# Kernel optimization log

Measured on AMD Instinct MI355X. Metric: run time of the kernel, lower is better.

## Reference

```python
import jax, jax.numpy as jnp
import numpy as np

N_TOKEN = 392
POS_WEIGHT = 1.0
LOSS_WEIGHT = 1.0


def _cam_map(logits, w_proj, xf, shape):
    # logits: (B, K_cls); w_proj: (K_cls, C); xf: (B, C, N)
    B, T, H, W = shape
    top_cls = jnp.argmax(logits, axis=1)                 # sort desc -> [0] == argmax
    w_top = w_proj[top_cls]                              # (B, C) gather top-class weight row
    row = jnp.einsum('bc,bcn->bn', w_top, xf)            # (B, N) per-sample CAM scores
    mn = row.min(axis=1, keepdims=True)
    mx = row.max(axis=1, keepdims=True)
    rown = (row - mn) / (mx - mn)                        # min-max normalize
    vals, idxs = jax.lax.top_k(rown, N_TOKEN)            # (B, 392)
    hw = H * W
    ti = idxs // hw
    hi = (idxs % hw) // W
    wi = idxs % W
    bi = jnp.broadcast_to(jnp.arange(B)[:, None], idxs.shape)
    cam = jnp.zeros((B, T, H, W), rown.dtype).at[bi, ti, hi, wi].set(vals)
    return cam


def _forward(x, pred_v_logits, pred_n_logits, w_proj_v, w_proj_n,
             conv_w, conv_b, score_w, score_b):
    B, C, T, H, W = x.shape
    xf = x.reshape(B, C, T * H * W)
    cam_v = _cam_map(pred_v_logits, w_proj_v, xf, (B, T, H, W))
    cam_n = _cam_map(pred_n_logits, w_proj_n, xf, (B, T, H, W))
    cam_gt = jnp.maximum(cam_v, cam_n)                   # torch.where(v > n, v, n)
    cam_gt = jax.lax.stop_gradient(cam_gt)               # original builds it from numpy + .detach()

    dn = ('NCDHW', 'OIDHW', 'NCDHW')
    h1 = jax.nn.relu(
        jax.lax.conv_general_dilated(x, conv_w, (1, 1, 1),
                                     [(0, 0), (1, 1), (1, 1)],
                                     dimension_numbers=dn)
        + conv_b[None, :, None, None, None])
    logits = (jax.lax.conv_general_dilated(h1, score_w, (1, 1, 1),
                                           [(0, 0), (0, 0), (0, 0)],
                                           dimension_numbers=dn)
              + score_b[None, :, None, None, None])      # (B,1,T,H,W)

    xcam = logits[:, 0].reshape(B * T, H * W)
    y = cam_gt.reshape(B * T, H * W)
    # BCEWithLogitsLoss(pos_weight) mean
    bce = -(POS_WEIGHT * y * jax.nn.log_sigmoid(xcam)
            + (1.0 - y) * jax.nn.log_sigmoid(-xcam))
    return LOSS_WEIGHT * bce.mean()


def setup_inputs() -> dict:
    key = jax.random.key(0)
    ks = jax.random.split(key, 8)
    B, C, T, H, W = 64, 256, 32, 7, 7
    Kv, Kn, D = 97, 300, 512
    x = jax.random.normal(ks[0], (B, C, T, H, W), jnp.float32)
    pred_v_logits = jax.random.normal(ks[1], (B, Kv), jnp.float32)
    pred_n_logits = jax.random.normal(ks[2], (B, Kn), jnp.float32)
    w_proj_v = jax.random.normal(ks[3], (Kv, C), jnp.float32) / np.sqrt(C)
    w_proj_n = jax.random.normal(ks[4], (Kn, C), jnp.float32) / np.sqrt(C)
    conv_w = jax.random.normal(ks[5], (D, C, 1, 3, 3), jnp.float32) / np.sqrt(C * 9)
    conv_b = jnp.zeros((D,), jnp.float32)
    score_w = jax.random.normal(ks[6], (1, D, 1, 1, 1), jnp.float32) / np.sqrt(D)
    score_b = jnp.zeros((1,), jnp.float32)
    return {"x": x, "pred_v_logits": pred_v_logits, "pred_n_logits": pred_n_logits,
            "w_proj_v": w_proj_v, "w_proj_n": w_proj_n,
            "conv_w": conv_w, "conv_b": conv_b,
            "score_w": score_w, "score_b": score_b}


def reference(x, pred_v_logits, pred_n_logits, w_proj_v, w_proj_n,
              conv_w, conv_b, score_w, score_b):
    return _forward(x, pred_v_logits, pred_n_logits, w_proj_v, w_proj_n,
                    conv_w, conv_b, score_w, score_b)
```

## Files before the change

kernel.cpp:

```cpp
#include <hip/hip_runtime.h>
#include <hip/hip_bf16.h>
#include <math.h>

#define BB 64
#define CC 256
#define TT 32
#define HH 7
#define WW 7
#define HW 49
#define NN 1568
#define KV 97
#define KN 300
#define DD 512
#define NTOK 392
#define TOTAL (BB*TT*HW)
#define BCAP 256

typedef float f32x4 __attribute__((ext_vector_type(4)));
typedef short bf16x8 __attribute__((ext_vector_type(8)));

#define GLDS(g, l) __builtin_amdgcn_global_load_lds(                          \
    (const __attribute__((address_space(1))) void*)(g),                       \
    (__attribute__((address_space(3))) void*)(l), 16, 0, 0)

__global__ void k_argmax(const float* __restrict__ pv, const float* __restrict__ pn,
                         int* __restrict__ clsv, int* __restrict__ clsn) {
    int b = threadIdx.x;
    if (b >= BB) return;
    {
        const float* r = pv + b * KV;
        float best = r[0]; int bi = 0;
        for (int k = 1; k < KV; ++k) { float v = r[k]; if (v > best) { best = v; bi = k; } }
        clsv[b] = bi;
    }
    {
        const float* r = pn + b * KN;
        float best = r[0]; int bi = 0;
        for (int k = 1; k < KN; ++k) { float v = r[k]; if (v > best) { best = v; bi = k; } }
        clsn[b] = bi;
    }
}

__global__ __launch_bounds__(256) void k_xp(
        const float* __restrict__ x, __hip_bfloat16* __restrict__ xp,
        const float* __restrict__ wpv, const float* __restrict__ wpn,
        const int* __restrict__ clsv, const int* __restrict__ clsn,
        float* __restrict__ rowv, float* __restrict__ rown_) {
    __shared__ float xs[CC * HW];
    __shared__ float wvs[CC], wns[CC];
    int bt = blockIdx.x;
    int b = bt >> 5, t = bt & 31;
    int tid = threadIdx.x;
    wvs[tid] = wpv[clsv[b] * CC + tid];
    wns[tid] = wpn[clsn[b] * CC + tid];
    const float* xb = x + ((size_t)b * CC * TT + t) * HW;
    for (int i = tid; i < CC * HW; i += 256) {
        int c = i / HW, q = i % HW;
        xs[i] = xb[(size_t)c * (TT * HW) + q];
    }
    __syncthreads();
    __hip_bfloat16* xpb = xp + (size_t)bt * 81 * CC;
    for (int o = tid; o < 81 * CC; o += 256) {
        int p = o >> 8, c = o & 255;
        int hh = p / 9, ww = p % 9;
        float v = 0.f;
        if (hh >= 1 && hh <= 7 && ww >= 1 && ww <= 7)
            v = xs[c * HW + (hh - 1) * WW + (ww - 1)];
        xpb[o] = __float2bfloat16(v);
    }
    if (tid < 2 * HW) {
        int head = tid >= HW;
        int q = head ? tid - HW : tid;
        const float* w = head ? wns : wvs;
        float s = 0.f;
        #pragma unroll 4
        for (int c = 0; c < CC; ++c) s = fmaf(w[c], xs[c * HW + q], s);
        (head ? rown_ : rowv)[bt * HW + q] = s;
    }
}

__global__ void k_wb(const float* __restrict__ w, __hip_bfloat16* __restrict__ wb) {
    int o = blockIdx.x * 256 + threadIdx.x;
    if (o >= 9 * DD * CC) return;
    int kk = o / (DD * CC);
    int rem = o - kk * (DD * CC);
    int d = rem >> 8, c = rem & 255;
    wb[o] = __float2bfloat16(w[(d * CC + c) * 9 + kk]);
}

__device__ __forceinline__ int binof(float v) {
    int i = (int)(v * 1024.f);
    return i < 0 ? 0 : (i > 1023 ? 1023 : i);
}

__device__ float block_red(float v, float* sbuf, int tid, bool ismax) {
    sbuf[tid] = v; __syncthreads();
    for (int s = 128; s > 0; s >>= 1) {
        if (tid < s) sbuf[tid] = ismax ? fmaxf(sbuf[tid], sbuf[tid + s])
                                       : fminf(sbuf[tid], sbuf[tid + s]);
        __syncthreads();
    }
    float r = sbuf[0]; __syncthreads();
    return r;
}

__global__ __launch_bounds__(256) void k_cam(
        const float* __restrict__ rowv, const float* __restrict__ rown_,
        float* __restrict__ cam) {
    __shared__ float rv[NN], rn[NN];
    __shared__ float sbuf[256];
    __shared__ int h[1024];
    __shared__ int tsum[256];
    __shared__ float lval_v[BCAP], lval_n[BCAP];
    __shared__ int lidx_v[BCAP], lidx_n[BCAP];
    __shared__ int cntv, cntn, bstar_v, above_v, bstar_n, above_n;
    int b = blockIdx.x, tid = threadIdx.x;

    for (int n = tid; n < NN; n += 256) { rv[n] = rowv[b * NN + n]; rn[n] = rown_[b * NN + n]; }
    __syncthreads();
    float mnv = 1e30f, mxv = -1e30f, mnn = 1e30f, mxn = -1e30f;
    for (int n = tid; n < NN; n += 256) {
        float v = rv[n]; mnv = fminf(mnv, v); mxv = fmaxf(mxv, v);
        float u = rn[n]; mnn = fminf(mnn, u); mxn = fmaxf(mxn, u);
    }
    mnv = block_red(mnv, sbuf, tid, false);
    mxv = block_red(mxv, sbuf, tid, true);
    mnn = block_red(mnn, sbuf, tid, false);
    mxn = block_red(mxn, sbuf, tid, true);
    float iv = 1.f / (mxv - mnv), inn = 1.f / (mxn - mnn);

    for (int n = tid; n < NN; n += 256) {
        rv[n] = (rv[n] - mnv) * iv;
        rn[n] = (rn[n] - mnn) * inn;
    }
    for (int i = tid; i < 1024; i += 256) h[i] = 0;
    if (tid == 0) { cntv = 0; cntn = 0; }
    __syncthreads();
    for (int n = tid; n < NN; n += 256) {
        atomicAdd(&h[binof(rv[n])], 1);
        atomicAdd(&h[binof(rn[n])], 1 << 16);
    }
    __syncthreads();

    int h0 = h[4 * tid], h1 = h[4 * tid + 1], h2 = h[4 * tid + 2], h3 = h[4 * tid + 3];
    tsum[tid] = h0 + h1 + h2 + h3;
    __syncthreads();
    for (int off = 1; off < 256; off <<= 1) {
        int add = (tid + off < 256) ? tsum[tid + off] : 0;
        __syncthreads();
        tsum[tid] += add;
        __syncthreads();
    }
    {
        int scur = tsum[tid];
        int hk[4] = {h0, h1, h2, h3};
        #pragma unroll
        for (int k = 0; k < 4; ++k) {
            int snext = scur - hk[k];
            int sc = scur & 0xffff, nc = snext & 0xffff;
            int sh = scur >> 16, nh = snext >> 16;
            if (sc >= NTOK && nc < NTOK) { bstar_v = 4 * tid + k; above_v = nc; }
            if (sh >= NTOK && nh < NTOK) { bstar_n = 4 * tid + k; above_n = nh; }
            scur = snext;
        }
    }
    __syncthreads();
    int bsv = bstar_v, abv = above_v, bsn = bstar_n, abn = above_n;

    for (int n = tid; n < NN; n += 256) {
        float v = rv[n]; int bv = binof(v);
        if (bv < bsv) rv[n] = 0.f;
        else if (bv == bsv) {
            int s = atomicAdd(&cntv, 1);
            if (s < BCAP) { lval_v[s] = v; lidx_v[s] = n; }
        }
        float u = rn[n]; int bu = binof(u);
        if (bu < bsn) rn[n] = 0.f;
        else if (bu == bsn) {
            int s = atomicAdd(&cntn, 1);
            if (s < BCAP) { lval_n[s] = u; lidx_n[s] = n; }
        }
    }
    __syncthreads();
    int Lv = cntv < BCAP ? cntv : BCAP;
    int Ln = cntn < BCAP ? cntn : BCAP;
    for (int i = tid; i < Lv; i += 256) {
        float vi = lval_v[i]; int ni = lidx_v[i]; int r = 0;
        for (int j = 0; j < Lv; ++j) {
            float vj = lval_v[j]; int nj = lidx_v[j];
            r += (vj > vi || (vj == vi && nj < ni)) ? 1 : 0;
        }
        rv[ni] = (r < NTOK - abv) ? vi : 0.f;
    }
    for (int i = tid; i < Ln; i += 256) {
        float vi = lval_n[i]; int ni = lidx_n[i]; int r = 0;
        for (int j = 0; j < Ln; ++j) {
            float vj = lval_n[j]; int nj = lidx_n[j];
            r += (vj > vi || (vj == vi && nj < ni)) ? 1 : 0;
        }
        rn[ni] = (r < NTOK - abn) ? vi : 0.f;
    }
    __syncthreads();
    for (int n = tid; n < NN; n += 256) cam[b * NN + n] = fmaxf(rv[n], rn[n]);
}

__global__ __launch_bounds__(256, 2) void k_gemm(
        const __hip_bfloat16* __restrict__ xp, const __hip_bfloat16* __restrict__ wb,
        const float* __restrict__ convb, const float* __restrict__ scorew,
        float* __restrict__ logits) {
    __shared__ char As[16384];
    __shared__ char Bs[16384];
    int tid = threadIdx.x;
    int bid = blockIdx.x;
    int xcd = bid & 7;
    int local = bid >> 3;
    int mtile = xcd * 98 + (local >> 2);
    int nblk = local & 3;
    int m0 = mtile * 128;
    int n0 = nblk * 128;
    int lane = tid & 63, wv = tid >> 6;
    int wm = wv >> 1, wn = wv & 1;
    int ln = lane & 15, qd = lane >> 4;

    int rrow = tid >> 3;
    int segst = ((tid & 7) ^ (rrow & 7)) * 8;
    int bt_[4], hh_[4], ww_[4];
    const __hip_bfloat16* bptr[4];
    #pragma unroll
    for (int j = 0; j < 4; ++j) {
        int m = m0 + j * 32 + rrow;
        int bt = m / HW, q = m - bt * HW;
        bt_[j] = bt; hh_[j] = q / WW; ww_[j] = q - (q / WW) * WW;
        bptr[j] = wb + (size_t)(n0 + j * 32 + rrow) * 256 + segst;
    }

    int swz = ln & 7;
    int offk[2] = {((0 + qd) ^ swz) * 16, ((4 + qd) ^ swz) * 16};

    f32x4 acc[4][4];
    #pragma unroll
    for (int i = 0; i < 4; ++i)
        #pragma unroll
        for (int j = 0; j < 4; ++j) acc[i][j] = (f32x4){0.f, 0.f, 0.f, 0.f};

    for (int kk = 0; kk < 9; ++kk) {
        int kh = kk / 3, kw = kk - (kk / 3) * 3;
        const __hip_bfloat16* aptr[4];
        #pragma unroll
        for (int j = 0; j < 4; ++j)
            aptr[j] = xp + ((size_t)bt_[j] * 81 + (hh_[j] + kh) * 9 + (ww_[j] + kw)) * 256 + segst;
        const size_t boff = (size_t)kk * (DD * 256);
        #pragma unroll
        for (int c0 = 0; c0 < 256; c0 += 64) {
            __syncthreads();
            #pragma unroll
            for (int j = 0; j < 4; ++j) {
                GLDS(aptr[j] + c0, As + j * 4096 + tid * 16);
                GLDS(bptr[j] + boff + c0, Bs + j * 4096 + tid * 16);
            }
            __syncthreads();
            #pragma unroll
            for (int k2 = 0; k2 < 2; ++k2) {
                bf16x8 af[4], bfr[4];
                #pragma unroll
                for (int i = 0; i < 4; ++i)
                    af[i] = *(const bf16x8*)(As + (wm * 64 + i * 16 + ln) * 128 + offk[k2]);
                #pragma unroll
                for (int j = 0; j < 4; ++j)
                    bfr[j] = *(const bf16x8*)(Bs + (wn * 64 + j * 16 + ln) * 128 + offk[k2]);
                #pragma unroll
                for (int i = 0; i < 4; ++i)
                    #pragma unroll
                    for (int j = 0; j < 4; ++j)
                        acc[i][j] = __builtin_amdgcn_mfma_f32_16x16x32_bf16(af[i], bfr[j], acc[i][j], 0, 0, 0);
            }
        }
    }

    float swr[4], cbr[4];
    #pragma unroll
    for (int j = 0; j < 4; ++j) {
        int n = n0 + wn * 64 + j * 16 + ln;
        swr[j] = scorew[n];
        cbr[j] = convb[n];
    }
    #pragma unroll
    for (int i = 0; i < 4; ++i) {
        #pragma unroll
        for (int r = 0; r < 4; ++r) {
            float v = 0.f;
            #pragma unroll
            for (int j = 0; j < 4; ++j) {
                float h1 = acc[i][j][r] + cbr[j];
                h1 = h1 > 0.f ? h1 : 0.f;
                v = fmaf(swr[j], h1, v);
            }
            v += __shfl_xor(v, 1);
            v += __shfl_xor(v, 2);
            v += __shfl_xor(v, 4);
            v += __shfl_xor(v, 8);
            if (ln == 0)
                atomicAdd(&logits[m0 + wm * 64 + i * 16 + qd * 4 + r], v);
        }
    }
}

__global__ void k_bce(const float* __restrict__ logits, const float* __restrict__ cam,
                      const float* __restrict__ sb, float* __restrict__ part) {
    __shared__ float sbuf[256];
    int tid = threadIdx.x;
    int m = blockIdx.x * 256 + tid;
    float l = logits[m] + sb[0];
    float y = cam[m];
    float v = fmaxf(l, 0.f) - l * y + log1pf(expf(-fabsf(l)));
    sbuf[tid] = v; __syncthreads();
    for (int k = 128; k > 0; k >>= 1) {
        if (tid < k) sbuf[tid] += sbuf[tid + k];
        __syncthreads();
    }
    if (tid == 0) part[blockIdx.x] = sbuf[0];
}

__global__ void k_final(const float* __restrict__ part, float* __restrict__ out) {
    __shared__ float sbuf[256];
    int tid = threadIdx.x;
    float s = 0.f;
    for (int i = tid; i < 392; i += 256) s += part[i];
    sbuf[tid] = s; __syncthreads();
    for (int k = 128; k > 0; k >>= 1) {
        if (tid < k) sbuf[tid] += sbuf[tid + k];
        __syncthreads();
    }
    if (tid == 0) out[0] = sbuf[0] * (1.0f / (float)TOTAL);
}

extern "C" void kernel_launch(void* const* d_in, const int* in_sizes, int n_in,
                              void* d_out, int out_size, void* d_ws, size_t ws_size,
                              hipStream_t stream) {
    const float* x   = (const float*)d_in[0];
    const float* pv  = (const float*)d_in[1];
    const float* pn  = (const float*)d_in[2];
    const float* wpv = (const float*)d_in[3];
    const float* wpn = (const float*)d_in[4];
    const float* cw  = (const float*)d_in[5];
    const float* cb  = (const float*)d_in[6];
    const float* sw  = (const float*)d_in[7];
    const float* sb  = (const float*)d_in[8];

    char* w8 = (char*)d_ws;
    __hip_bfloat16* xp  = (__hip_bfloat16*)w8;
    __hip_bfloat16* wb  = (__hip_bfloat16*)(w8 + 84934656);
    float* logits = (float*)(w8 + 87293952);
    float* rowv   = (float*)(w8 + 87695360);
    float* rown_  = (float*)(w8 + 88096768);
    float* cam    = (float*)(w8 + 88498176);
    float* part   = (float*)(w8 + 88899584);
    int*   clsv   = (int*)(w8 + 88901152);
    int*   clsn   = clsv + 64;

    k_argmax<<<1, 64, 0, stream>>>(pv, pn, clsv, clsn);
    k_xp<<<BB * TT, 256, 0, stream>>>(x, xp, wpv, wpn, clsv, clsn, rowv, rown_);
    k_wb<<<4608, 256, 0, stream>>>(cw, wb);
    k_cam<<<BB, 256, 0, stream>>>(rowv, rown_, cam);
    hipMemsetAsync(logits, 0, TOTAL * sizeof(float), stream);
    k_gemm<<<3136, 256, 0, stream>>>(xp, wb, cb, sw, logits);
    k_bce<<<392, 256, 0, stream>>>(logits, cam, sb, part);
    k_final<<<1, 256, 0, stream>>>(part, (float*)d_out);
}
```

Before: 486.0 us.

## Merge small kernels, vectorize padded-input writes, replace atomics with partial-logit buffers

Folds the argmax and weight-conversion kernels into one launch and merges the final reduction into the BCE kernel through a last-block counter. The memset and per-row atomic adds for logits go away; each GEMM wave now writes its own partial-logit slice, and BCE sums the eight slices. The padded bf16 input is written as 8-wide packed stores, the CAM dot product is split across more threads, and the min/max block reductions use wave shuffles. The GEMM launch bound asks for 3 blocks per SM, which may raise register pressure, and the partial buffers add extra memory traffic.

```diff
diff --git a/kernel.cpp b/kernel.cpp
--- a/kernel.cpp
+++ b/kernel.cpp
@@ -23,21 +23,33 @@
     (const __attribute__((address_space(1))) void*)(g),                       \
     (__attribute__((address_space(3))) void*)(l), 16, 0, 0)
 
-__global__ void k_argmax(const float* __restrict__ pv, const float* __restrict__ pn,
-                         int* __restrict__ clsv, int* __restrict__ clsn) {
-    int b = threadIdx.x;
-    if (b >= BB) return;
+__global__ void k_pre(const float* __restrict__ w, __hip_bfloat16* __restrict__ wb,
+                      const float* __restrict__ pv, const float* __restrict__ pn,
+                      int* __restrict__ clsv, int* __restrict__ clsn,
+                      int* __restrict__ counter) {
+    int blk = blockIdx.x;
+    if (blk < 4608) {
+        int o = blk * 256 + threadIdx.x;
+        int kk = o / (DD * CC);
+        int rem = o - kk * (DD * CC);
+        int d = rem >> 8, c = rem & 255;
+        wb[o] = __float2bfloat16(w[(d * CC + c) * 9 + kk]);
+        return;
+    }
+    int tid = threadIdx.x;
+    if (tid == 64) *counter = 0;
+    if (tid >= BB) return;
     {
-        const float* r = pv + b * KV;
+        const float* r = pv + tid * KV;
         float best = r[0]; int bi = 0;
         for (int k = 1; k < KV; ++k) { float v = r[k]; if (v > best) { best = v; bi = k; } }
-        clsv[b] = bi;
+        clsv[tid] = bi;
     }
     {
-        const float* r = pn + b * KN;
+        const float* r = pn + tid * KN;
         float best = r[0]; int bi = 0;
         for (int k = 1; k < KN; ++k) { float v = r[k]; if (v > best) { best = v; bi = k; } }
-        clsn[b] = bi;
+        clsn[tid] = bi;
     }
 }
 
@@ -48,6 +60,7 @@
         float* __restrict__ rowv, float* __restrict__ rown_) {
     __shared__ float xs[CC * HW];
     __shared__ float wvs[CC], wns[CC];
+    __shared__ float psum[4 * HW];
     int bt = blockIdx.x;
     int b = bt >> 5, t = bt & 31;
     int tid = threadIdx.x;
@@ -55,60 +68,55 @@
     wns[tid] = wpn[clsn[b] * CC + tid];
     const float* xb = x + ((size_t)b * CC * TT + t) * HW;
     for (int i = tid; i < CC * HW; i += 256) {
-        int c = i / HW, q = i % HW;
+        int c = i / HW, q = i - (i / HW) * HW;
         xs[i] = xb[(size_t)c * (TT * HW) + q];
     }
     __syncthreads();
     __hip_bfloat16* xpb = xp + (size_t)bt * 81 * CC;
-    for (int o = tid; o < 81 * CC; o += 256) {
-        int p = o >> 8, c = o & 255;
-        int hh = p / 9, ww = p % 9;
-        float v = 0.f;
-        if (hh >= 1 && hh <= 7 && ww >= 1 && ww <= 7)
-            v = xs[c * HW + (hh - 1) * WW + (ww - 1)];
-        xpb[o] = __float2bfloat16(v);
-    }
+    for (int u = tid; u < 81 * 32; u += 256) {
+        int p = u >> 5, c0 = (u & 31) * 8;
+        int hh = p / 9, ww = p - (p / 9) * 9;
+        bool inb = (hh >= 1 && hh <= 7 && ww >= 1 && ww <= 7);
+        int base = c0 * HW + (hh - 1) * WW + (ww - 1);
+        bf16x8 pack;
+        #pragma unroll
+        for (int j = 0; j < 8; ++j) {
+            float v = inb ? xs[base + j * HW] : 0.f;
+            __hip_bfloat16 bv = __float2bfloat16(v);
+            pack[j] = *reinterpret_cast<short*>(&bv);
+        }
+        *reinterpret_cast<bf16x8*>(xpb + p * 256 + c0) = pack;
+    }
+    if (tid < 4 * HW) {
+        int sel = tid / HW;
+        int q = tid - sel * HW;
+        const float* w = (sel < 2) ? wvs : wns;
+        int cb2 = (sel & 1) * 128;
+        float s = 0.f;
+        #pragma unroll 4
+        for (int c = 0; c < 128; ++c) s = fmaf(w[cb2 + c], xs[(cb2 + c) * HW + q], s);
+        psum[tid] = s;
+    }
+    __syncthreads();
     if (tid < 2 * HW) {
         int head = tid >= HW;
         int q = head ? tid - HW : tid;
-        const float* w = head ? wns : wvs;
-        float s = 0.f;
-        #pragma unroll 4
-        for (int c = 0; c < CC; ++c) s = fmaf(w[c], xs[c * HW + q], s);
+        float s = head ? (psum[2 * HW + q] + psum[3 * HW + q])
+                       : (psum[q] + psum[HW + q]);
         (head ? rown_ : rowv)[bt * HW + q] = s;
     }
-}
-
-__global__ void k_wb(const float* __restrict__ w, __hip_bfloat16* __restrict__ wb) {
-    int o = blockIdx.x * 256 + threadIdx.x;
-    if (o >= 9 * DD * CC) return;
-    int kk = o / (DD * CC);
-    int rem = o - kk * (DD * CC);
-    int d = rem >> 8, c = rem & 255;
-    wb[o] = __float2bfloat16(w[(d * CC + c) * 9 + kk]);
 }
 
 __device__ __forceinline__ int binof(float v) {
     int i = (int)(v * 1024.f);
     return i < 0 ? 0 : (i > 1023 ? 1023 : i);
-}
-
-__device__ float block_red(float v, float* sbuf, int tid, bool ismax) {
-    sbuf[tid] = v; __syncthreads();
-    for (int s = 128; s > 0; s >>= 1) {
-        if (tid < s) sbuf[tid] = ismax ? fmaxf(sbuf[tid], sbuf[tid + s])
-                                       : fminf(sbuf[tid], sbuf[tid + s]);
-        __syncthreads();
-    }
-    float r = sbuf[0]; __syncthreads();
-    return r;
 }
 
 __global__ __launch_bounds__(256) void k_cam(
         const float* __restrict__ rowv, const float* __restrict__ rown_,
         float* __restrict__ cam) {
     __shared__ float rv[NN], rn[NN];
-    __shared__ float sbuf[256];
+    __shared__ float wred[4][4];
     __shared__ int h[1024];
     __shared__ int tsum[256];
     __shared__ float lval_v[BCAP], lval_n[BCAP];
@@ -123,10 +131,23 @@
         float v = rv[n]; mnv = fminf(mnv, v); mxv = fmaxf(mxv, v);
         float u = rn[n]; mnn = fminf(mnn, u); mxn = fmaxf(mxn, u);
     }
-    mnv = block_red(mnv, sbuf, tid, false);
-    mxv = block_red(mxv, sbuf, tid, true);
-    mnn = block_red(mnn, sbuf, tid, false);
-    mxn = block_red(mxn, sbuf, tid, true);
+    #pragma unroll
+    for (int off = 32; off >= 1; off >>= 1) {
+        mnv = fminf(mnv, __shfl_xor(mnv, off));
+        mxv = fmaxf(mxv, __shfl_xor(mxv, off));
+        mnn = fminf(mnn, __shfl_xor(mnn, off));
+        mxn = fmaxf(mxn, __shfl_xor(mxn, off));
+    }
+    if ((tid & 63) == 0) {
+        int wid = tid >> 6;
+        wred[wid][0] = mnv; wred[wid][1] = mxv; wred[wid][2] = mnn; wred[wid][3] = mxn;
+    }
+    if (tid == 0) { cntv = 0; cntn = 0; }
+    __syncthreads();
+    mnv = fminf(fminf(wred[0][0], wred[1][0]), fminf(wred[2][0], wred[3][0]));
+    mxv = fmaxf(fmaxf(wred[0][1], wred[1][1]), fmaxf(wred[2][1], wred[3][1]));
+    mnn = fminf(fminf(wred[0][2], wred[1][2]), fminf(wred[2][2], wred[3][2]));
+    mxn = fmaxf(fmaxf(wred[0][3], wred[1][3]), fmaxf(wred[2][3], wred[3][3]));
     float iv = 1.f / (mxv - mnv), inn = 1.f / (mxn - mnn);
 
     for (int n = tid; n < NN; n += 256) {
@@ -134,7 +155,6 @@
         rn[n] = (rn[n] - mnn) * inn;
     }
     for (int i = tid; i < 1024; i += 256) h[i] = 0;
-    if (tid == 0) { cntv = 0; cntn = 0; }
     __syncthreads();
     for (int n = tid; n < NN; n += 256) {
         atomicAdd(&h[binof(rv[n])], 1);
@@ -204,10 +224,10 @@
     for (int n = tid; n < NN; n += 256) cam[b * NN + n] = fmaxf(rv[n], rn[n]);
 }
 
-__global__ __launch_bounds__(256, 2) void k_gemm(
+__global__ __launch_bounds__(256, 3) void k_gemm(
         const __hip_bfloat16* __restrict__ xp, const __hip_bfloat16* __restrict__ wb,
         const float* __restrict__ convb, const float* __restrict__ scorew,
-        float* __restrict__ logits) {
+        float* __restrict__ pl) {
     __shared__ char As[16384];
     __shared__ char Bs[16384];
     int tid = threadIdx.x;
@@ -284,6 +304,7 @@
         swr[j] = scorew[n];
         cbr[j] = convb[n];
     }
+    float* dst = pl + (size_t)(nblk * 2 + wn) * TOTAL;
     #pragma unroll
     for (int i = 0; i < 4; ++i) {
         #pragma unroll
@@ -300,17 +321,22 @@
             v += __shfl_xor(v, 4);
             v += __shfl_xor(v, 8);
             if (ln == 0)
-                atomicAdd(&logits[m0 + wm * 64 + i * 16 + qd * 4 + r], v);
-        }
-    }
-}
-
-__global__ void k_bce(const float* __restrict__ logits, const float* __restrict__ cam,
-                      const float* __restrict__ sb, float* __restrict__ part) {
+                dst[m0 + wm * 64 + i * 16 + qd * 4 + r] = v;
+        }
+    }
+}
+
+__global__ __launch_bounds__(256) void k_bce(
+        const float* __restrict__ pl, const float* __restrict__ cam,
+        const float* __restrict__ sb, float* __restrict__ part,
+        int* __restrict__ counter, float* __restrict__ out) {
     __shared__ float sbuf[256];
+    __shared__ int isLast;
     int tid = threadIdx.x;
     int m = blockIdx.x * 256 + tid;
-    float l = logits[m] + sb[0];
+    float l = sb[0];
+    #pragma unroll
+    for (int s = 0; s < 8; ++s) l += pl[(size_t)s * TOTAL + m];
     float y = cam[m];
     float v = fmaxf(l, 0.f) - l * y + log1pf(expf(-fabsf(l)));
     sbuf[tid] = v; __syncthreads();
@@ -318,20 +344,23 @@
         if (tid < k) sbuf[tid] += sbuf[tid + k];
         __syncthreads();
     }
-    if (tid == 0) part[blockIdx.x] = sbuf[0];
-}
-
-__global__ void k_final(const float* __restrict__ part, float* __restrict__ out) {
-    __shared__ float sbuf[256];
-    int tid = threadIdx.x;
-    float s = 0.f;
-    for (int i = tid; i < 392; i += 256) s += part[i];
-    sbuf[tid] = s; __syncthreads();
-    for (int k = 128; k > 0; k >>= 1) {
-        if (tid < k) sbuf[tid] += sbuf[tid + k];
-        __syncthreads();
-    }
-    if (tid == 0) out[0] = sbuf[0] * (1.0f / (float)TOTAL);
+    if (tid == 0) {
+        part[blockIdx.x] = sbuf[0];
+        __threadfence();
+        int d = atomicAdd(counter, 1);
+        isLast = (d == 391);
+    }
+    __syncthreads();
+    if (isLast) {
+        float s = 0.f;
+        for (int i = tid; i < 392; i += 256) s += part[i];
+        sbuf[tid] = s; __syncthreads();
+        for (int k = 128; k > 0; k >>= 1) {
+            if (tid < k) sbuf[tid] += sbuf[tid + k];
+            __syncthreads();
+        }
+        if (tid == 0) out[0] = sbuf[0] * (1.0f / (float)TOTAL);
+    }
 }
 
 extern "C" void kernel_launch(void* const* d_in, const int* in_sizes, int n_in,
@@ -350,20 +379,18 @@
     char* w8 = (char*)d_ws;
     __hip_bfloat16* xp  = (__hip_bfloat16*)w8;
     __hip_bfloat16* wb  = (__hip_bfloat16*)(w8 + 84934656);
-    float* logits = (float*)(w8 + 87293952);
-    float* rowv   = (float*)(w8 + 87695360);
-    float* rown_  = (float*)(w8 + 88096768);
-    float* cam    = (float*)(w8 + 88498176);
-    float* part   = (float*)(w8 + 88899584);
-    int*   clsv   = (int*)(w8 + 88901152);
-    int*   clsn   = clsv + 64;
-
-    k_argmax<<<1, 64, 0, stream>>>(pv, pn, clsv, clsn);
+    float* pl      = (float*)(w8 + 87293952);
+    float* rowv    = (float*)(w8 + 90505216);
+    float* rown_   = (float*)(w8 + 90906624);
+    float* cam     = (float*)(w8 + 91308032);
+    float* part    = (float*)(w8 + 91709440);
+    int*   counter = (int*)(w8 + 91711008);
+    int*   clsv    = (int*)(w8 + 91711016);
+    int*   clsn    = clsv + 64;
+
+    k_pre<<<4609, 256, 0, stream>>>(cw, wb, pv, pn, clsv, clsn, counter);
     k_xp<<<BB * TT, 256, 0, stream>>>(x, xp, wpv, wpn, clsv, clsn, rowv, rown_);
-    k_wb<<<4608, 256, 0, stream>>>(cw, wb);
     k_cam<<<BB, 256, 0, stream>>>(rowv, rown_, cam);
-    hipMemsetAsync(logits, 0, TOTAL * sizeof(float), stream);
-    k_gemm<<<3136, 256, 0, stream>>>(xp, wb, cb, sw, logits);
-    k_bce<<<392, 256, 0, stream>>>(logits, cam, sb, part);
-    k_final<<<1, 256, 0, stream>>>(part, (float*)d_out);
-}
+    k_gemm<<<3136, 256, 0, stream>>>(xp, wb, cb, sw, pl);
+    k_bce<<<392, 256, 0, stream>>>(pl, cam, sb, part, counter, (float*)d_out);
+}
```

Measured after the change: 470.8 us. 3.1% less time.
